# Kernel tuning notes

Measured on AMD Instinct MI355X. Metric: run time of the kernel, lower is better.

## Reference

```python
import jax, jax.numpy as jnp
import numpy as np

B, N, C = 4, 1370, 1024
H, DH = 16, C // 16
N_ROPE = 1369  # patch tokens covered by RoPE (prefix=1 CLS token)


def _rotate_half(x):
    x1, x2 = jnp.split(x, 2, axis=-1)
    return jnp.concatenate([-x2, x1], axis=-1)


def _rope_apply(x, sin, cos):
    return x * cos + _rotate_half(x) * sin


def setup_inputs() -> dict:
    key = jax.random.key(0)
    ks = jax.random.split(key, 7)
    return {
        "x": jax.random.normal(ks[0], (B, N, C), dtype=jnp.float32),
        "sin": jax.random.normal(ks[1], (N_ROPE, DH), dtype=jnp.float32),
        "cos": jax.random.normal(ks[2], (N_ROPE, DH), dtype=jnp.float32),
        "w_qkv": jax.random.normal(ks[3], (C, 3 * C), dtype=jnp.float32) * (C ** -0.5),
        "b_qkv": jax.random.normal(ks[4], (3 * C,), dtype=jnp.float32) * 0.02,
        "w_proj": jax.random.normal(ks[5], (C, C), dtype=jnp.float32) * (C ** -0.5),
        "b_proj": jax.random.normal(ks[6], (C,), dtype=jnp.float32) * 0.02,
    }


def reference(x, sin, cos, w_qkv, b_qkv, w_proj, b_proj):
    b, n, c = x.shape
    # QKV projection -> [3, B, H, N, DH]
    qkv = (x @ w_qkv + b_qkv).reshape(b, n, 3, H, DH).transpose(2, 0, 3, 1, 4)
    q, k, v = qkv[0], qkv[1], qkv[2]
    # RoPE on the last N_ROPE tokens (prefix tokens, e.g. CLS, left untouched)
    prefix = n - sin.shape[-2]
    q = jnp.concatenate([q[:, :, :prefix, :], _rope_apply(q[:, :, prefix:, :], sin, cos)], axis=-2)
    k = jnp.concatenate([k[:, :, :prefix, :], _rope_apply(k[:, :, prefix:, :], sin, cos)], axis=-2)
    # Full attention
    scale = 1.0 / jnp.sqrt(jnp.asarray(DH, dtype=x.dtype))
    attn = jnp.einsum('bhqd,bhkd->bhqk', q, k) * scale
    attn = jax.nn.softmax(attn, axis=-1)
    out = jnp.einsum('bhqk,bhkd->bhqd', attn, v)
    out = out.transpose(0, 2, 1, 3).reshape(b, n, c)
    return out @ w_proj + b_proj
```

## Files before the change

kernel.cpp:

```cpp
#include <hip/hip_runtime.h>
#include <hip/hip_bf16.h>

#define B_ 4
#define N_ 1370
#define C_ 1024
#define H_ 16
#define DH_ 64
#define NR_ 1369
#define M_ (B_*N_)
#define VTS_ 1408
#define ALS 64
#define PLS 72

#define QSCALE 0.1803368801111f

typedef _Float16 f16x8  __attribute__((ext_vector_type(8)));
typedef __bf16   bf16x8 __attribute__((ext_vector_type(8)));
typedef float    f32x4  __attribute__((ext_vector_type(4)));

__device__ __forceinline__ f16x8 ld_frag_h(const unsigned short* p) {
    uint4 u = *(const uint4*)p;
    return __builtin_bit_cast(f16x8, u);
}
__device__ __forceinline__ bf16x8 ld_frag_b(const unsigned short* p) {
    uint4 u = *(const uint4*)p;
    return __builtin_bit_cast(bf16x8, u);
}
__device__ __forceinline__ unsigned short f2h(float f) {
    _Float16 h = (_Float16)f;
    return __builtin_bit_cast(unsigned short, h);
}
__device__ __forceinline__ unsigned short f2bf(float f) {
    __hip_bfloat16 h = __float2bfloat16(f);
    return __builtin_bit_cast(unsigned short, h);
}
__device__ __forceinline__ bf16x8 ones_bf() {
    uint4 u = make_uint4(0x3F803F80u, 0x3F803F80u, 0x3F803F80u, 0x3F803F80u);
    return __builtin_bit_cast(bf16x8, u);
}

__device__ __forceinline__ void load_lds16(const unsigned short* g, unsigned short* l) {
    __builtin_amdgcn_global_load_lds(
        (const __attribute__((address_space(1))) unsigned int*)g,
        (__attribute__((address_space(3))) unsigned int*)l,
        16, 0, 0);
}

__global__ __launch_bounds__(256)
void conv_x_k(const float* __restrict__ x, unsigned short* __restrict__ xo, int total4) {
    int i = blockIdx.x * 256 + threadIdx.x;
    if (i >= total4) return;
    float4 v = ((const float4*)x)[i];
    ushort4 h;
    h.x = f2h(v.x); h.y = f2h(v.y); h.z = f2h(v.z); h.w = f2h(v.w);
    ((ushort4*)xo)[i] = h;
}

__global__ __launch_bounds__(256)
void conv_wt_k(const float* __restrict__ w, unsigned short* __restrict__ wt, int Ncol) {
    __shared__ unsigned short Th[64][68];
    const int tid = threadIdx.x, tx = tid & 15, ty = tid >> 4;
    const int k0 = blockIdx.y * 64, n0 = blockIdx.x * 64;
    #pragma unroll
    for (int i = 0; i < 4; ++i) {
        const int k = ty + i * 16;
        float4 v = *(const float4*)&w[(size_t)(k0 + k) * Ncol + n0 + tx * 4];
        Th[k][tx*4+0] = f2h(v.x); Th[k][tx*4+1] = f2h(v.y);
        Th[k][tx*4+2] = f2h(v.z); Th[k][tx*4+3] = f2h(v.w);
    }
    __syncthreads();
    #pragma unroll
    for (int i = 0; i < 4; ++i) {
        const int n = ty + i * 16;
        ushort4 o;
        o.x = Th[tx*4+0][n]; o.y = Th[tx*4+1][n]; o.z = Th[tx*4+2][n]; o.w = Th[tx*4+3][n];
        *(ushort4*)&wt[(size_t)(n0 + n) * 1024 + k0 + tx * 4] = o;
    }
}

template<int MODE, int MT>
__global__ __launch_bounds__(256)
void gemm_mfma(const unsigned short* __restrict__ A, const unsigned short* __restrict__ Bt,
               const float* __restrict__ bias, float* __restrict__ out,
               unsigned short* __restrict__ qb, unsigned short* __restrict__ kb,
               unsigned short* __restrict__ vtb,
               const float* __restrict__ sinp, const float* __restrict__ cosp,
               int nchunks)
{
    constexpr int MI = MT / 32;
    __shared__ __align__(16) unsigned short A_s[MT * 64];
    __shared__ __align__(16) unsigned short B_s[128 * 64];

    const int tid = threadIdx.x;
    const int wave = tid >> 6, lane = tid & 63;
    const int quad = lane >> 4, l16 = lane & 15;
    const int m0 = blockIdx.y * MT, n0 = blockIdx.x * 128;
    const int mwave = (wave & 1) * (MT / 2), nwave = (wave >> 1) * 64;

    const int srow = lane >> 3;
    const int gseg = (lane & 7) ^ srow;

    f32x4 acc[MI][4] = {};

    for (int kc = 0; kc < nchunks; ++kc) {
        const int kof = kc * 64;

        __syncthreads();
        #pragma unroll
        for (int i = 0; i < MI; ++i) {
            const int rbase = wave * (8 * MI) + i * 8;
            int arow = m0 + rbase + srow;
            if (arow > M_ - 1) arow = M_ - 1;
            load_lds16(A + (size_t)arow * 1024 + kof + gseg * 8, &A_s[rbase * 64]);
        }
        #pragma unroll
        for (int i = 0; i < 4; ++i) {
            const int rbase = wave * 32 + i * 8;
            const int brow = n0 + rbase + srow;
            load_lds16(Bt + (size_t)brow * 1024 + kof + gseg * 8, &B_s[rbase * 64]);
        }
        __syncthreads();

        #pragma unroll
        for (int kh = 0; kh < 2; ++kh) {
            const int soff = (((kh * 4 + quad) ^ (l16 & 7)) << 3);
            f16x8 a[MI], b[4];
            #pragma unroll
            for (int t = 0; t < MI; ++t)
                a[t] = ld_frag_h(&A_s[(mwave + t * 16 + l16) * 64 + soff]);
            #pragma unroll
            for (int t = 0; t < 4; ++t)
                b[t] = ld_frag_h(&B_s[(nwave + t * 16 + l16) * 64 + soff]);
            #pragma unroll
            for (int i = 0; i < MI; ++i)
                #pragma unroll
                for (int j = 0; j < 4; ++j)
                    acc[i][j] = __builtin_amdgcn_mfma_f32_16x16x32_f16(a[i], b[j], acc[i][j], 0, 0, 0);
        }
    }

    if (MODE == 0) {
        #pragma unroll
        for (int i = 0; i < MI; ++i) {
            #pragma unroll
            for (int r = 0; r < 4; ++r) {
                const int gm = m0 + mwave + i * 16 + quad * 4 + r;
                if (gm >= M_) continue;
                #pragma unroll
                for (int j = 0; j < 4; ++j) {
                    const int gn = n0 + nwave + j * 16 + l16;
                    out[(size_t)gm * 1024 + gn] = acc[i][j][r] + bias[gn];
                }
            }
        }
    } else {
        const int part = n0 >> 10;
        #pragma unroll
        for (int i = 0; i < MI; ++i) {
            #pragma unroll
            for (int r = 0; r < 4; ++r) {
                const int gm = m0 + mwave + i * 16 + quad * 4 + r;
                if (gm >= M_) continue;
                const int b = gm / N_;
                const int tok = gm - b * N_;

                float val[4];
                #pragma unroll
                for (int j = 0; j < 4; ++j) {
                    const int gn = n0 + nwave + j * 16 + l16;
                    val[j] = acc[i][j][r] + bias[gn];
                }

                if (part < 2 && tok >= 1) {
                    const float* sp = sinp + (size_t)(tok - 1) * DH_;
                    const float* cp = cosp + (size_t)(tok - 1) * DH_;
                    const float s0 = sp[l16],      s1 = sp[16 + l16];
                    const float s2 = sp[32 + l16], s3 = sp[48 + l16];
                    const float c0 = cp[l16],      c1 = cp[16 + l16];
                    const float c2 = cp[32 + l16], c3 = cp[48 + l16];
                    const float n0v = fmaf(val[0], c0, -val[2] * s0);
                    const float n1v = fmaf(val[1], c1, -val[3] * s1);
                    const float n2v = fmaf(val[2], c2,  val[0] * s2);
                    const float n3v = fmaf(val[3], c3,  val[1] * s3);
                    val[0] = n0v; val[1] = n1v; val[2] = n2v; val[3] = n3v;
                }

                #pragma unroll
                for (int j = 0; j < 4; ++j) {
                    const int gn = n0 + nwave + j * 16 + l16;
                    const int cc = gn & 1023;
                    const int h = cc >> 6, d = cc & 63;
                    const int bh = b * H_ + h;
                    if (part == 0)      qb[((size_t)bh * N_ + tok) * DH_ + d] = f2h(val[j] * QSCALE);
                    else if (part == 1) kb[((size_t)bh * N_ + tok) * DH_ + d] = f2h(val[j]);
                    else                vtb[((size_t)bh * DH_ + d) * VTS_ + tok] = f2bf(val[j]);
                }
            }
        }
    }
}

__global__ __launch_bounds__(256)
void attn_k(const unsigned short* __restrict__ q, const unsigned short* __restrict__ k,
            const unsigned short* __restrict__ vt, unsigned short* __restrict__ out)
{
    __shared__ __align__(16) unsigned short Ks[2][64 * ALS];
    __shared__ __align__(16) unsigned short Vs[2][64 * ALS];
    __shared__ __align__(16) unsigned short Ps[4 * 32 * PLS];

    const int tid  = threadIdx.x;
    const int wave = tid >> 6, lane = tid & 63;
    const int quad = lane >> 4, l16 = lane & 15;
    const int srow = lane >> 3;
    const int gseg = (lane & 7) ^ srow;
    const int bh = blockIdx.y;
    const int q0 = blockIdx.x * 128;

    const unsigned short* qp  = q  + (size_t)bh * N_ * DH_;
    const unsigned short* kp  = k  + (size_t)bh * N_ * DH_;
    const unsigned short* vtp = vt + (size_t)bh * DH_ * VTS_;

    f16x8 qf[2][2];
    #pragma unroll
    for (int s = 0; s < 2; ++s) {
        int qrow = q0 + wave * 32 + s * 16 + l16;
        if (qrow > N_ - 1) qrow = N_ - 1;
        qf[s][0] = ld_frag_h(qp + (size_t)qrow * DH_ + quad * 8);
        qf[s][1] = ld_frag_h(qp + (size_t)qrow * DH_ + 32 + quad * 8);
    }

    const bf16x8 onesv = ones_bf();
    f32x4 O[2][4] = {};
    f32x4 L[2] = {};

    unsigned short* Pw = Ps + wave * 32 * PLS;
    const int so0 = ((quad)     ^ (l16 & 7)) << 3;
    const int so1 = ((4 + quad) ^ (l16 & 7)) << 3;

    auto stage = [&](int ch, int buf) {
        const int k0 = ch * 64;
        #pragma unroll
        for (int i = 0; i < 2; ++i) {
            const int rbase = wave * 16 + i * 8;
            int krow = k0 + rbase + srow;
            if (krow > N_ - 1) krow = N_ - 1;
            load_lds16(kp + (size_t)krow * DH_ + gseg * 8, &Ks[buf][rbase * ALS]);
            load_lds16(vtp + (size_t)(rbase + srow) * VTS_ + k0 + gseg * 8, &Vs[buf][rbase * ALS]);
        }
    };

    stage(0, 0);

    for (int ch = 0; ch < 22; ++ch) {
        const int k0 = ch * 64;
        const int cur = ch & 1;
        __syncthreads();
        if (ch + 1 < 22) stage(ch + 1, 1 - cur);

        f16x8 kf[4][2];
        #pragma unroll
        for (int t = 0; t < 4; ++t) {
            kf[t][0] = ld_frag_h(&Ks[cur][(t * 16 + l16) * ALS + so0]);
            kf[t][1] = ld_frag_h(&Ks[cur][(t * 16 + l16) * ALS + so1]);
        }
        f32x4 S[2][4];
        #pragma unroll
        for (int s = 0; s < 2; ++s) {
            #pragma unroll
            for (int t = 0; t < 4; ++t) {
                f32x4 z = {};
                z = __builtin_amdgcn_mfma_f32_16x16x32_f16(qf[s][0], kf[t][0], z, 0, 0, 0);
                z = __builtin_amdgcn_mfma_f32_16x16x32_f16(qf[s][1], kf[t][1], z, 0, 0, 0);
                S[s][t] = z;
            }
        }
        if (k0 + 64 > N_) {
            #pragma unroll
            for (int t = 0; t < 4; ++t) {
                if (k0 + t * 16 + l16 >= N_) {
                    #pragma unroll
                    for (int s = 0; s < 2; ++s) {
                        S[s][t][0] = -1e30f; S[s][t][1] = -1e30f;
                        S[s][t][2] = -1e30f; S[s][t][3] = -1e30f;
                    }
                }
            }
        }

        #pragma unroll
        for (int s = 0; s < 2; ++s) {
            #pragma unroll
            for (int t = 0; t < 4; ++t) {
                #pragma unroll
                for (int r = 0; r < 4; ++r) {
                    const float p = __builtin_amdgcn_exp2f(S[s][t][r]);
                    Pw[(s * 16 + quad * 4 + r) * PLS + t * 16 + l16] = f2bf(p);
                }
            }
        }
        __builtin_amdgcn_wave_barrier();

        bf16x8 pf[2][2];
        #pragma unroll
        for (int s = 0; s < 2; ++s) {
            pf[s][0] = ld_frag_b(&Pw[(s * 16 + l16) * PLS + quad * 8]);
            pf[s][1] = ld_frag_b(&Pw[(s * 16 + l16) * PLS + 32 + quad * 8]);
        }
        bf16x8 vf[4][2];
        #pragma unroll
        for (int dt = 0; dt < 4; ++dt) {
            vf[dt][0] = ld_frag_b(&Vs[cur][(dt * 16 + l16) * ALS + so0]);
            vf[dt][1] = ld_frag_b(&Vs[cur][(dt * 16 + l16) * ALS + so1]);
        }
        #pragma unroll
        for (int s = 0; s < 2; ++s) {
            L[s] = __builtin_amdgcn_mfma_f32_16x16x32_bf16(pf[s][0], onesv, L[s], 0, 0, 0);
            L[s] = __builtin_amdgcn_mfma_f32_16x16x32_bf16(pf[s][1], onesv, L[s], 0, 0, 0);
            #pragma unroll
            for (int dt = 0; dt < 4; ++dt) {
                O[s][dt] = __builtin_amdgcn_mfma_f32_16x16x32_bf16(pf[s][0], vf[dt][0], O[s][dt], 0, 0, 0);
                O[s][dt] = __builtin_amdgcn_mfma_f32_16x16x32_bf16(pf[s][1], vf[dt][1], O[s][dt], 0, 0, 0);
            }
        }
    }

    const int b = bh >> 4, h = bh & 15;
    #pragma unroll
    for (int s = 0; s < 2; ++s) {
        #pragma unroll
        for (int r = 0; r < 4; ++r) {
            const int qi = q0 + wave * 32 + s * 16 + quad * 4 + r;
            if (qi < N_) {
                const float inv = 1.0f / L[s][r];
                unsigned short* op = out + ((size_t)(b * N_ + qi)) * C_ + h * DH_ + l16;
                #pragma unroll
                for (int dt = 0; dt < 4; ++dt) op[dt * 16] = f2h(O[s][dt][r] * inv);
            }
        }
    }
}

extern "C" void kernel_launch(void* const* d_in, const int* in_sizes, int n_in,
                              void* d_out, int out_size, void* d_ws, size_t ws_size,
                              hipStream_t stream) {
    const float* x      = (const float*)d_in[0];
    const float* sinp   = (const float*)d_in[1];
    const float* cosp   = (const float*)d_in[2];
    const float* w_qkv  = (const float*)d_in[3];
    const float* b_qkv  = (const float*)d_in[4];
    const float* w_proj = (const float*)d_in[5];
    const float* b_proj = (const float*)d_in[6];
    float* out = (float*)d_out;

    unsigned short* p = (unsigned short*)d_ws;
    const size_t xsz  = (size_t)M_ * C_;
    const size_t wqsz = (size_t)3 * C_ * C_;
    const size_t wpsz = (size_t)C_ * C_;
    const size_t hsz  = (size_t)B_ * H_ * N_ * DH_;
    const size_t vtsz = (size_t)B_ * H_ * DH_ * VTS_;
    unsigned short* x_h   = p;            p += xsz;
    unsigned short* wq_t  = p;            p += wqsz;
    unsigned short* wp_t  = p;            p += wpsz;
    unsigned short* q     = p;            p += hsz;
    unsigned short* k     = p;            p += hsz;
    unsigned short* vt    = p;            p += vtsz;
    unsigned short* attnb = p;            p += xsz;

    conv_x_k<<<(int)((xsz / 4 + 255) / 256), 256, 0, stream>>>(x, x_h, (int)(xsz / 4));
    conv_wt_k<<<dim3(3 * C_ / 64, C_ / 64), 256, 0, stream>>>(w_qkv, wq_t, 3 * C_);
    conv_wt_k<<<dim3(C_ / 64, C_ / 64), 256, 0, stream>>>(w_proj, wp_t, C_);

    gemm_mfma<1, 128><<<dim3(3 * C_ / 128, (M_ + 127) / 128), 256, 0, stream>>>(
        x_h, wq_t, b_qkv, nullptr, q, k, vt, sinp, cosp, 16);

    attn_k<<<dim3((N_ + 127) / 128, B_ * H_), 256, 0, stream>>>(q, k, vt, attnb);

    gemm_mfma<0, 64><<<dim3(C_ / 128, (M_ + 63) / 64), 256, 0, stream>>>(
        attnb, wp_t, b_proj, out, nullptr, nullptr, nullptr, nullptr, nullptr, 16);
}
```

Before: 259.9 us.

## Load attention K/V fragments directly from global and pack RoPE sin/cos

The attention kernel stops staging K and V^T tiles into double-buffered LDS with async global-to-LDS loads and block barriers. Each wave now reads its MFMA fragments straight from global memory, relying on cache hits across the four waves. Separately, sin/cos are repacked into a per-lane interleaved float layout during the x conversion kernel, so the QKV GEMM epilogue reads two float4 vectors instead of eight scalar loads. The K/V change drops syncthreads and LDS traffic, but it raises redundant global and L2 traffic and loses the load/compute overlap that double buffering provided.

```diff
diff --git a/kernel.cpp b/kernel.cpp
--- a/kernel.cpp
+++ b/kernel.cpp
@@ -9,7 +9,6 @@
 #define NR_ 1369
 #define M_ (B_*N_)
 #define VTS_ 1408
-#define ALS 64
 #define PLS 72
 
 #define QSCALE 0.1803368801111f
@@ -47,13 +46,25 @@
 }
 
 __global__ __launch_bounds__(256)
-void conv_x_k(const float* __restrict__ x, unsigned short* __restrict__ xo, int total4) {
+void conv_x_k(const float* __restrict__ x, unsigned short* __restrict__ xo, int total4,
+              const float* __restrict__ sinp, const float* __restrict__ cosp,
+              float* __restrict__ scpack) {
     int i = blockIdx.x * 256 + threadIdx.x;
-    if (i >= total4) return;
-    float4 v = ((const float4*)x)[i];
-    ushort4 h;
-    h.x = f2h(v.x); h.y = f2h(v.y); h.z = f2h(v.z); h.w = f2h(v.w);
-    ((ushort4*)xo)[i] = h;
+    if (i < total4) {
+        float4 v = ((const float4*)x)[i];
+        ushort4 h;
+        h.x = f2h(v.x); h.y = f2h(v.y); h.z = f2h(v.z); h.w = f2h(v.w);
+        ((ushort4*)xo)[i] = h;
+        return;
+    }
+    int j = i - total4;
+    if (j >= NR_ * 16) return;
+    const int tok1 = j >> 4, l16 = j & 15;
+    float* o = scpack + (size_t)j * 8;
+    const float* sp = sinp + (size_t)tok1 * DH_;
+    const float* cp = cosp + (size_t)tok1 * DH_;
+    o[0] = sp[l16]; o[1] = sp[16 + l16]; o[2] = sp[32 + l16]; o[3] = sp[48 + l16];
+    o[4] = cp[l16]; o[5] = cp[16 + l16]; o[6] = cp[32 + l16]; o[7] = cp[48 + l16];
 }
 
 __global__ __launch_bounds__(256)
@@ -84,7 +95,7 @@
                const float* __restrict__ bias, float* __restrict__ out,
                unsigned short* __restrict__ qb, unsigned short* __restrict__ kb,
                unsigned short* __restrict__ vtb,
-               const float* __restrict__ sinp, const float* __restrict__ cosp,
+               const float* __restrict__ scpack,
                int nchunks)
 {
     constexpr int MI = MT / 32;
@@ -172,16 +183,13 @@
                 }
 
                 if (part < 2 && tok >= 1) {
-                    const float* sp = sinp + (size_t)(tok - 1) * DH_;
-                    const float* cp = cosp + (size_t)(tok - 1) * DH_;
-                    const float s0 = sp[l16],      s1 = sp[16 + l16];
-                    const float s2 = sp[32 + l16], s3 = sp[48 + l16];
-                    const float c0 = cp[l16],      c1 = cp[16 + l16];
-                    const float c2 = cp[32 + l16], c3 = cp[48 + l16];
-                    const float n0v = fmaf(val[0], c0, -val[2] * s0);
-                    const float n1v = fmaf(val[1], c1, -val[3] * s1);
-                    const float n2v = fmaf(val[2], c2,  val[0] * s2);
-                    const float n3v = fmaf(val[3], c3,  val[1] * s3);
+                    const float* scp = scpack + (((size_t)(tok - 1)) * 16 + l16) * 8;
+                    float4 sv = *(const float4*)scp;
+                    float4 cv = *(const float4*)(scp + 4);
+                    const float n0v = fmaf(val[0], cv.x, -val[2] * sv.x);
+                    const float n1v = fmaf(val[1], cv.y, -val[3] * sv.y);
+                    const float n2v = fmaf(val[2], cv.z,  val[0] * sv.z);
+                    const float n3v = fmaf(val[3], cv.w,  val[1] * sv.w);
                     val[0] = n0v; val[1] = n1v; val[2] = n2v; val[3] = n3v;
                 }
 
@@ -204,15 +212,11 @@
 void attn_k(const unsigned short* __restrict__ q, const unsigned short* __restrict__ k,
             const unsigned short* __restrict__ vt, unsigned short* __restrict__ out)
 {
-    __shared__ __align__(16) unsigned short Ks[2][64 * ALS];
-    __shared__ __align__(16) unsigned short Vs[2][64 * ALS];
     __shared__ __align__(16) unsigned short Ps[4 * 32 * PLS];
 
     const int tid  = threadIdx.x;
     const int wave = tid >> 6, lane = tid & 63;
     const int quad = lane >> 4, l16 = lane & 15;
-    const int srow = lane >> 3;
-    const int gseg = (lane & 7) ^ srow;
     const int bh = blockIdx.y;
     const int q0 = blockIdx.x * 128;
 
@@ -234,34 +238,17 @@
     f32x4 L[2] = {};
 
     unsigned short* Pw = Ps + wave * 32 * PLS;
-    const int so0 = ((quad)     ^ (l16 & 7)) << 3;
-    const int so1 = ((4 + quad) ^ (l16 & 7)) << 3;
-
-    auto stage = [&](int ch, int buf) {
-        const int k0 = ch * 64;
-        #pragma unroll
-        for (int i = 0; i < 2; ++i) {
-            const int rbase = wave * 16 + i * 8;
-            int krow = k0 + rbase + srow;
-            if (krow > N_ - 1) krow = N_ - 1;
-            load_lds16(kp + (size_t)krow * DH_ + gseg * 8, &Ks[buf][rbase * ALS]);
-            load_lds16(vtp + (size_t)(rbase + srow) * VTS_ + k0 + gseg * 8, &Vs[buf][rbase * ALS]);
-        }
-    };
-
-    stage(0, 0);
 
     for (int ch = 0; ch < 22; ++ch) {
         const int k0 = ch * 64;
-        const int cur = ch & 1;
-        __syncthreads();
-        if (ch + 1 < 22) stage(ch + 1, 1 - cur);
 
         f16x8 kf[4][2];
         #pragma unroll
         for (int t = 0; t < 4; ++t) {
-            kf[t][0] = ld_frag_h(&Ks[cur][(t * 16 + l16) * ALS + so0]);
-            kf[t][1] = ld_frag_h(&Ks[cur][(t * 16 + l16) * ALS + so1]);
+            int krow = k0 + t * 16 + l16;
+            if (krow > N_ - 1) krow = N_ - 1;
+            kf[t][0] = ld_frag_h(kp + (size_t)krow * DH_ + quad * 8);
+            kf[t][1] = ld_frag_h(kp + (size_t)krow * DH_ + 32 + quad * 8);
         }
         f32x4 S[2][4];
         #pragma unroll
@@ -309,8 +296,9 @@
         bf16x8 vf[4][2];
         #pragma unroll
         for (int dt = 0; dt < 4; ++dt) {
-            vf[dt][0] = ld_frag_b(&Vs[cur][(dt * 16 + l16) * ALS + so0]);
-            vf[dt][1] = ld_frag_b(&Vs[cur][(dt * 16 + l16) * ALS + so1]);
+            const unsigned short* vrow = vtp + (size_t)(dt * 16 + l16) * VTS_ + k0;
+            vf[dt][0] = ld_frag_b(vrow + quad * 8);
+            vf[dt][1] = ld_frag_b(vrow + 32 + quad * 8);
         }
         #pragma unroll
         for (int s = 0; s < 2; ++s) {
@@ -365,16 +353,19 @@
     unsigned short* k     = p;            p += hsz;
     unsigned short* vt    = p;            p += vtsz;
     unsigned short* attnb = p;            p += xsz;
-
-    conv_x_k<<<(int)((xsz / 4 + 255) / 256), 256, 0, stream>>>(x, x_h, (int)(xsz / 4));
+    float* scpack = (float*)(p + (p - (unsigned short*)d_ws) % 2);
+
+    const int total4 = (int)(xsz / 4);
+    const int convblocks = (total4 + NR_ * 16 + 255) / 256;
+    conv_x_k<<<convblocks, 256, 0, stream>>>(x, x_h, total4, sinp, cosp, scpack);
     conv_wt_k<<<dim3(3 * C_ / 64, C_ / 64), 256, 0, stream>>>(w_qkv, wq_t, 3 * C_);
     conv_wt_k<<<dim3(C_ / 64, C_ / 64), 256, 0, stream>>>(w_proj, wp_t, C_);
 
     gemm_mfma<1, 128><<<dim3(3 * C_ / 128, (M_ + 127) / 128), 256, 0, stream>>>(
-        x_h, wq_t, b_qkv, nullptr, q, k, vt, sinp, cosp, 16);
+        x_h, wq_t, b_qkv, nullptr, q, k, vt, scpack, 16);
 
     attn_k<<<dim3((N_ + 127) / 128, B_ * H_), 256, 0, stream>>>(q, k, vt, attnb);
 
     gemm_mfma<0, 64><<<dim3(C_ / 128, (M_ + 63) / 64), 256, 0, stream>>>(
-        attnb, wp_t, b_proj, out, nullptr, nullptr, nullptr, nullptr, nullptr, 16);
-}
+        attnb, wp_t, b_proj, out, nullptr, nullptr, nullptr, nullptr, 16);
+}
```

New measurement: 339.5 us. +30.6%, slower.
